# Kernel tuning notes

Measured on AMD Instinct MI355X. Metric: run time of the kernel, lower is better.

The kernel has to match this reference:

```python
import jax, jax.numpy as jnp
import numpy as np

B, T, F = 64, 128, 9            # batch, seq_len, n_feature_fields
N_FEATURES = 32000              # vocab for embedding (N_FEATURES-1 rows) and fc head
EMB = 8
H = 16                          # lstm hidden size
IN0 = (F - 1) * EMB + 1         # lstm layer-0 input size = 65


def setup_inputs() -> dict:
    key = jax.random.key(0)
    ks = jax.random.split(key, 16)
    # x: first F-1 columns are integer-valued categorical indices, last column numeric
    cat = jax.random.randint(ks[0], (B, T, F - 1), 0, N_FEATURES - 1).astype(jnp.float32)
    num = jax.random.normal(ks[1], (B, T, 1), dtype=jnp.float32)
    x = jnp.concatenate([cat, num], axis=-1)
    h0 = jnp.zeros((2, B, H), dtype=jnp.float32)
    c0 = jnp.zeros((2, B, H), dtype=jnp.float32)
    emb = jax.random.normal(ks[2], (N_FEATURES - 1, EMB), dtype=jnp.float32)
    s0 = 1.0 / np.sqrt(IN0)
    s1 = 1.0 / np.sqrt(H)
    W_ih0 = jax.random.normal(ks[3], (4 * H, IN0), dtype=jnp.float32) * s0
    W_hh0 = jax.random.normal(ks[4], (4 * H, H), dtype=jnp.float32) * s1
    b_ih0 = jax.random.normal(ks[5], (4 * H,), dtype=jnp.float32) * 0.1
    b_hh0 = jax.random.normal(ks[6], (4 * H,), dtype=jnp.float32) * 0.1
    W_ih1 = jax.random.normal(ks[7], (4 * H, H), dtype=jnp.float32) * s1
    W_hh1 = jax.random.normal(ks[8], (4 * H, H), dtype=jnp.float32) * s1
    b_ih1 = jax.random.normal(ks[9], (4 * H,), dtype=jnp.float32) * 0.1
    b_hh1 = jax.random.normal(ks[10], (4 * H,), dtype=jnp.float32) * 0.1
    fc_w = jax.random.normal(ks[11], (N_FEATURES, H), dtype=jnp.float32) * (1.0 / np.sqrt(H))
    fc_b = jax.random.normal(ks[12], (N_FEATURES,), dtype=jnp.float32) * 0.1
    return {"x": x, "h0": h0, "c0": c0, "emb": emb,
            "W_ih0": W_ih0, "W_hh0": W_hh0, "b_ih0": b_ih0, "b_hh0": b_hh0,
            "W_ih1": W_ih1, "W_hh1": W_hh1, "b_ih1": b_ih1, "b_hh1": b_hh1,
            "fc_w": fc_w, "fc_b": fc_b}


def _lstm_layer(xs, h0, c0, Wih, Whh, bih, bhh):
    # xs: [B, T, I]; PyTorch gate order: i, f, g, o
    xp = jnp.einsum('bti,gi->btg', xs, Wih) + (bih + bhh)  # [B, T, 4H]
    xp = jnp.swapaxes(xp, 0, 1)  # [T, B, 4H]

    def step(carry, xt):
        h, c = carry
        g = xt + h @ Whh.T
        i, f, gg, o = jnp.split(g, 4, axis=-1)
        c = jax.nn.sigmoid(f) * c + jax.nn.sigmoid(i) * jnp.tanh(gg)
        h = jax.nn.sigmoid(o) * jnp.tanh(c)
        return (h, c), h

    (hT, cT), ys = jax.lax.scan(step, (h0, c0), xp)
    return jnp.swapaxes(ys, 0, 1), hT, cT


def reference(x, h0, c0, emb, W_ih0, W_hh0, b_ih0, b_hh0,
              W_ih1, W_hh1, b_ih1, b_hh1, fc_w, fc_b):
    cat = x[:, :, :-1].astype(jnp.int32)          # [B, T, F-1]
    num = x[:, :, -1:]                            # [B, T, 1]
    e = emb[cat].reshape(x.shape[0], x.shape[1], -1)  # [B, T, (F-1)*EMB]
    inp = jnp.concatenate([e, num], axis=-1)      # [B, T, IN0]
    y0, h0T, c0T = _lstm_layer(inp, h0[0], c0[0], W_ih0, W_hh0, b_ih0, b_hh0)
    y1, h1T, c1T = _lstm_layer(y0, h0[1], c0[1], W_ih1, W_hh1, b_ih1, b_hh1)
    logits = jnp.einsum('bth,vh->btv', y1, fc_w) + fc_b  # [B, T, N_FEATURES]
    hN = jnp.stack([h0T, h1T], axis=0)
    cN = jnp.stack([c0T, c1T], axis=0)
    return logits, hN, cN
```

## Files before the change

kernel.cpp:

```cpp
#include <hip/hip_runtime.h>
#include <math.h>

#define BB 64
#define TT 128
#define HH 16
#define GG 64
#define IN0_ 65
#define VV 32000
#define NROWS (BB*TT)
#define RSTRIDE 68

typedef float f32x4 __attribute__((ext_vector_type(4)));

__device__ __forceinline__ float sigf(float x) {
    return 1.0f / (1.0f + __expf(-x));
}
__device__ __forceinline__ float tanhfast(float x) {
    return 1.0f - 2.0f / (__expf(2.0f * x) + 1.0f);
}
__device__ __forceinline__ float bcast(float v, int lane) {
    return __uint_as_float(__builtin_amdgcn_readlane(__float_as_uint(v), lane));
}

__global__ __launch_bounds__(256) void fused_front(const float* __restrict__ x,
                           const float* __restrict__ emb,
                           const float* __restrict__ Wih0, const float* __restrict__ bih0,
                           const float* __restrict__ bhh0,
                           const float* __restrict__ h0in, const float* __restrict__ c0in,
                           const float* __restrict__ Whh0,
                           const float* __restrict__ Wih1, const float* __restrict__ Whh1,
                           const float* __restrict__ bih1, const float* __restrict__ bhh1,
                           float* __restrict__ y1, float* __restrict__ outTail) {
    __shared__ float insh[TT * RSTRIDE];
    __shared__ float wsh[GG * IN0_];
    const int b   = blockIdx.x;
    const int tid = threadIdx.x;
    const int wave = tid >> 6, g = tid & 63;
    const float* xb = x + (size_t)b * TT * 9;

    for (int i = tid; i < GG * IN0_ / 4; i += 256) {
        float4 wv = *reinterpret_cast<const float4*>(Wih0 + i * 4);
        wsh[i*4+0] = wv.x; wsh[i*4+1] = wv.y; wsh[i*4+2] = wv.z; wsh[i*4+3] = wv.w;
    }
    #pragma unroll
    for (int it = 0; it < 8; ++it) {
        int q = tid + it * 256;
        int p = q >> 1, half = q & 1;
        int r = p >> 3, f = p & 7;
        int idx = (int)xb[r * 9 + f];
        const float* er = emb + (size_t)idx * 8 + half * 4;
        float4 e = *reinterpret_cast<const float4*>(er);
        float* d = &insh[r * RSTRIDE + f * 8 + half * 4];
        d[0] = e.x; d[1] = e.y; d[2] = e.z; d[3] = e.w;
    }
    if (tid < TT) insh[tid * RSTRIDE + 64] = xb[tid * 9 + 8];
    __syncthreads();

    {
        float wreg[IN0_];
        #pragma unroll
        for (int k = 0; k < IN0_; ++k) wreg[k] = wsh[g * IN0_ + k];
        const float bias0 = bih0[g] + bhh0[g];
        for (int r = 0; r < 32; ++r) {
            const int row = wave * 32 + r;
            const float* ir = &insh[row * RSTRIDE];
            float a0 = bias0, a1 = 0.0f, a2 = 0.0f, a3 = 0.0f;
            #pragma unroll
            for (int k4 = 0; k4 < 16; ++k4) {
                f32x4 v = *reinterpret_cast<const f32x4*>(ir + k4 * 4);
                float p0 = v.x * wreg[k4*4+0] + v.y * wreg[k4*4+1]
                         + v.z * wreg[k4*4+2] + v.w * wreg[k4*4+3];
                if ((k4 & 3) == 0) a0 += p0;
                else if ((k4 & 3) == 1) a1 += p0;
                else if ((k4 & 3) == 2) a2 += p0;
                else a3 += p0;
            }
            float acc = (a0 + a1) + (a2 + a3) + ir[64] * wreg[64];
            insh[row * RSTRIDE + g] = acc;
        }
    }
    __syncthreads();

    if (tid >= 64) return;

    const int j = g & 15;
    float w0[HH], wi1[HH], w1[HH];
    #pragma unroll
    for (int k = 0; k < HH; ++k) {
        w0[k]  = Whh0[g * HH + k];
        wi1[k] = Wih1[g * HH + k];
        w1[k]  = Whh1[g * HH + k];
    }
    const float bias1 = bih1[g] + bhh1[g];

    float h0v = h0in[b * HH + j];
    float h1v = h0in[BB * HH + b * HH + j];
    float c0v = c0in[b * HH + j];
    float c1v = c0in[BB * HH + b * HH + j];

    {
        float aa = insh[g], ab = 0.0f;
        #pragma unroll
        for (int k = 0; k < 8; ++k) {
            aa += bcast(h0v, k) * w0[k];
            ab += bcast(h0v, k + 8) * w0[k + 8];
        }
        float acc = aa + ab;
        float iv = __shfl(acc, j), fv = __shfl(acc, j + 16);
        float gv = __shfl(acc, j + 32), ov = __shfl(acc, j + 48);
        c0v = sigf(fv) * c0v + sigf(iv) * tanhfast(gv);
        h0v = sigf(ov) * tanhfast(c0v);
    }

    for (int t = 0; t < TT - 1; ++t) {
        float xpn = insh[(t + 1) * RSTRIDE + g];
        float a1a = bias1, a1b = 0.0f, a1c = 0.0f, a1d = 0.0f;
        float a0a = 0.0f,  a0b = 0.0f;
        #pragma unroll
        for (int k = 0; k < 8; ++k) {
            float h0k  = bcast(h0v, k);
            float h0k8 = bcast(h0v, k + 8);
            float h1k  = bcast(h1v, k);
            float h1k8 = bcast(h1v, k + 8);
            a1a += h0k  * wi1[k];
            a1b += h0k8 * wi1[k + 8];
            a1c += h1k  * w1[k];
            a1d += h1k8 * w1[k + 8];
            a0a += h0k  * w0[k];
            a0b += h0k8 * w0[k + 8];
        }
        float acc1 = (a1a + a1b) + (a1c + a1d);
        float acc0 = xpn + a0a + a0b;
        float iv1 = __shfl(acc1, j), fv1 = __shfl(acc1, j + 16);
        float gv1 = __shfl(acc1, j + 32), ov1 = __shfl(acc1, j + 48);
        float iv0 = __shfl(acc0, j), fv0 = __shfl(acc0, j + 16);
        float gv0 = __shfl(acc0, j + 32), ov0 = __shfl(acc0, j + 48);
        c1v = sigf(fv1) * c1v + sigf(iv1) * tanhfast(gv1);
        h1v = sigf(ov1) * tanhfast(c1v);
        c0v = sigf(fv0) * c0v + sigf(iv0) * tanhfast(gv0);
        h0v = sigf(ov0) * tanhfast(c0v);
        if (g < HH) y1[(size_t)(b * TT + t) * HH + g] = h1v;
    }

    {
        float a1a = bias1, a1b = 0.0f, a1c = 0.0f, a1d = 0.0f;
        #pragma unroll
        for (int k = 0; k < 8; ++k) {
            float h0k  = bcast(h0v, k);
            float h0k8 = bcast(h0v, k + 8);
            float h1k  = bcast(h1v, k);
            float h1k8 = bcast(h1v, k + 8);
            a1a += h0k  * wi1[k];
            a1b += h0k8 * wi1[k + 8];
            a1c += h1k  * w1[k];
            a1d += h1k8 * w1[k + 8];
        }
        float acc1 = (a1a + a1b) + (a1c + a1d);
        float iv1 = __shfl(acc1, j), fv1 = __shfl(acc1, j + 16);
        float gv1 = __shfl(acc1, j + 32), ov1 = __shfl(acc1, j + 48);
        c1v = sigf(fv1) * c1v + sigf(iv1) * tanhfast(gv1);
        h1v = sigf(ov1) * tanhfast(c1v);
        if (g < HH) y1[(size_t)(b * TT + TT - 1) * HH + g] = h1v;
    }

    if (g < HH) {
        outTail[b * HH + g]               = h0v;
        outTail[BB * HH + b * HH + g]     = h1v;
        outTail[2 * BB * HH + b * HH + g] = c0v;
        outTail[3 * BB * HH + b * HH + g] = c1v;
    }
}

__global__ __launch_bounds__(256) void fc_kernel(const float* __restrict__ y1,
                          const float* __restrict__ fcw, const float* __restrict__ fcb,
                          float* __restrict__ out) {
    const int tid  = threadIdx.x;
    const int v0   = blockIdx.x * 1024 + tid * 4;
    const int row0 = blockIdx.y * 32;

    if (v0 >= VV) return;

    float w[4][HH];
    #pragma unroll
    for (int jj = 0; jj < 4; ++jj) {
        const float4* wp = reinterpret_cast<const float4*>(fcw + (size_t)(v0 + jj) * HH);
        float4 a = wp[0], b = wp[1], c = wp[2], d = wp[3];
        w[jj][0]=a.x; w[jj][1]=a.y; w[jj][2]=a.z; w[jj][3]=a.w;
        w[jj][4]=b.x; w[jj][5]=b.y; w[jj][6]=b.z; w[jj][7]=b.w;
        w[jj][8]=c.x; w[jj][9]=c.y; w[jj][10]=c.z; w[jj][11]=c.w;
        w[jj][12]=d.x; w[jj][13]=d.y; w[jj][14]=d.z; w[jj][15]=d.w;
    }
    const float4 bias = *reinterpret_cast<const float4*>(fcb + v0);

    const f32x4* yrow = reinterpret_cast<const f32x4*>(y1 + (size_t)row0 * HH);

    float* orow = out + (size_t)row0 * VV + v0;
    #pragma unroll 4
    for (int r = 0; r < 32; ++r) {
        f32x4 y0 = yrow[r * 4 + 0];
        f32x4 y1v = yrow[r * 4 + 1];
        f32x4 y2 = yrow[r * 4 + 2];
        f32x4 y3 = yrow[r * 4 + 3];
        float a0 = bias.x, a1 = bias.y, a2 = bias.z, a3 = bias.w;
        #pragma unroll
        for (int jj = 0; jj < 4; ++jj) {
            float* wj = w[jj];
            float acc = y0.x*wj[0] + y0.y*wj[1] + y0.z*wj[2] + y0.w*wj[3]
                      + y1v.x*wj[4] + y1v.y*wj[5] + y1v.z*wj[6] + y1v.w*wj[7]
                      + y2.x*wj[8] + y2.y*wj[9] + y2.z*wj[10] + y2.w*wj[11]
                      + y3.x*wj[12] + y3.y*wj[13] + y3.z*wj[14] + y3.w*wj[15];
            if (jj == 0) a0 += acc;
            else if (jj == 1) a1 += acc;
            else if (jj == 2) a2 += acc;
            else a3 += acc;
        }
        f32x4 o;
        o.x = a0; o.y = a1; o.z = a2; o.w = a3;
        __builtin_nontemporal_store(o, reinterpret_cast<f32x4*>(orow));
        orow += VV;
    }
}

extern "C" void kernel_launch(void* const* d_in, const int* in_sizes, int n_in,
                              void* d_out, int out_size, void* d_ws, size_t ws_size,
                              hipStream_t stream) {
    const float* x    = (const float*)d_in[0];
    const float* h0   = (const float*)d_in[1];
    const float* c0   = (const float*)d_in[2];
    const float* emb  = (const float*)d_in[3];
    const float* Wih0 = (const float*)d_in[4];
    const float* Whh0 = (const float*)d_in[5];
    const float* bih0 = (const float*)d_in[6];
    const float* bhh0 = (const float*)d_in[7];
    const float* Wih1 = (const float*)d_in[8];
    const float* Whh1 = (const float*)d_in[9];
    const float* bih1 = (const float*)d_in[10];
    const float* bhh1 = (const float*)d_in[11];
    const float* fcw  = (const float*)d_in[12];
    const float* fcb  = (const float*)d_in[13];

    float* out = (float*)d_out;
    float* y1  = (float*)d_ws;
    float* outTail = out + (size_t)NROWS * VV;

    fused_front<<<BB, 256, 0, stream>>>(x, emb, Wih0, bih0, bhh0, h0, c0,
                                        Whh0, Wih1, Whh1, bih1, bhh1, y1, outTail);
    fc_kernel<<<dim3(32, NROWS / 32), 256, 0, stream>>>(y1, fcw, fcb, out);
}
```

Baseline: 282.5 us.

## Process two batch sequences per block in fused LSTM front kernel

Each block of the fused embedding+LSTM kernel now handles two batch elements instead of one, interleaving their recurrences in a single wave. This gives the serial per-timestep chain independent work to hide readlane/shuffle/transcendental latency. The cost is half as many blocks, doubled LDS via dynamic shared memory (about 86KB), and more registers. Layer-0 input projection work per wave doubles.

New measurement: 346.5 us. 1.23x slower.

```diff
diff --git a/kernel.cpp b/kernel.cpp
--- a/kernel.cpp
+++ b/kernel.cpp
@@ -9,6 +9,7 @@
 #define VV 32000
 #define NROWS (BB*TT)
 #define RSTRIDE 68
+#define BOFF (TT*RSTRIDE)
 
 typedef float f32x4 __attribute__((ext_vector_type(4)));
 
@@ -31,29 +32,29 @@
                            const float* __restrict__ Wih1, const float* __restrict__ Whh1,
                            const float* __restrict__ bih1, const float* __restrict__ bhh1,
                            float* __restrict__ y1, float* __restrict__ outTail) {
-    __shared__ float insh[TT * RSTRIDE];
-    __shared__ float wsh[GG * IN0_];
-    const int b   = blockIdx.x;
+    extern __shared__ float smem[];
+    float* wsh = smem + 2 * BOFF;
+    const int b0  = blockIdx.x * 2;
     const int tid = threadIdx.x;
     const int wave = tid >> 6, g = tid & 63;
-    const float* xb = x + (size_t)b * TT * 9;
+    const float* xg = x + (size_t)b0 * TT * 9;
 
     for (int i = tid; i < GG * IN0_ / 4; i += 256) {
         float4 wv = *reinterpret_cast<const float4*>(Wih0 + i * 4);
         wsh[i*4+0] = wv.x; wsh[i*4+1] = wv.y; wsh[i*4+2] = wv.z; wsh[i*4+3] = wv.w;
     }
     #pragma unroll
-    for (int it = 0; it < 8; ++it) {
+    for (int it = 0; it < 16; ++it) {
         int q = tid + it * 256;
         int p = q >> 1, half = q & 1;
         int r = p >> 3, f = p & 7;
-        int idx = (int)xb[r * 9 + f];
+        int idx = (int)xg[r * 9 + f];
         const float* er = emb + (size_t)idx * 8 + half * 4;
         float4 e = *reinterpret_cast<const float4*>(er);
-        float* d = &insh[r * RSTRIDE + f * 8 + half * 4];
+        float* d = &smem[(r >> 7) * BOFF + (r & 127) * RSTRIDE + f * 8 + half * 4];
         d[0] = e.x; d[1] = e.y; d[2] = e.z; d[3] = e.w;
     }
-    if (tid < TT) insh[tid * RSTRIDE + 64] = xb[tid * 9 + 8];
+    smem[(tid >> 7) * BOFF + (tid & 127) * RSTRIDE + 64] = xg[tid * 9 + 8];
     __syncthreads();
 
     {
@@ -61,9 +62,10 @@
         #pragma unroll
         for (int k = 0; k < IN0_; ++k) wreg[k] = wsh[g * IN0_ + k];
         const float bias0 = bih0[g] + bhh0[g];
-        for (int r = 0; r < 32; ++r) {
-            const int row = wave * 32 + r;
-            const float* ir = &insh[row * RSTRIDE];
+        float* base = smem + (wave >> 1) * BOFF;
+        for (int r = 0; r < 64; ++r) {
+            const int row = (wave & 1) * 64 + r;
+            const float* ir = &base[row * RSTRIDE];
             float a0 = bias0, a1 = 0.0f, a2 = 0.0f, a3 = 0.0f;
             #pragma unroll
             for (int k4 = 0; k4 < 16; ++k4) {
@@ -76,7 +78,7 @@
                 else a3 += p0;
             }
             float acc = (a0 + a1) + (a2 + a3) + ir[64] * wreg[64];
-            insh[row * RSTRIDE + g] = acc;
+            base[row * RSTRIDE + g] = acc;
         }
     }
     __syncthreads();
@@ -92,82 +94,123 @@
         w1[k]  = Whh1[g * HH + k];
     }
     const float bias1 = bih1[g] + bhh1[g];
-
-    float h0v = h0in[b * HH + j];
-    float h1v = h0in[BB * HH + b * HH + j];
-    float c0v = c0in[b * HH + j];
-    float c1v = c0in[BB * HH + b * HH + j];
+    const int bA = b0, bB = b0 + 1;
+
+    float h0A = h0in[bA * HH + j],            h0B = h0in[bB * HH + j];
+    float h1A = h0in[BB * HH + bA * HH + j],  h1B = h0in[BB * HH + bB * HH + j];
+    float c0A = c0in[bA * HH + j],            c0B = c0in[bB * HH + j];
+    float c1A = c0in[BB * HH + bA * HH + j],  c1B = c0in[BB * HH + bB * HH + j];
+
+    const float* xpA = smem;
+    const float* xpB = smem + BOFF;
 
     {
-        float aa = insh[g], ab = 0.0f;
+        float aA = xpA[g], abA = 0.0f, aB = xpB[g], abB = 0.0f;
         #pragma unroll
         for (int k = 0; k < 8; ++k) {
-            aa += bcast(h0v, k) * w0[k];
-            ab += bcast(h0v, k + 8) * w0[k + 8];
-        }
-        float acc = aa + ab;
-        float iv = __shfl(acc, j), fv = __shfl(acc, j + 16);
-        float gv = __shfl(acc, j + 32), ov = __shfl(acc, j + 48);
-        c0v = sigf(fv) * c0v + sigf(iv) * tanhfast(gv);
-        h0v = sigf(ov) * tanhfast(c0v);
+            float wA = w0[k], wB = w0[k + 8];
+            aA  += bcast(h0A, k)     * wA;
+            abA += bcast(h0A, k + 8) * wB;
+            aB  += bcast(h0B, k)     * wA;
+            abB += bcast(h0B, k + 8) * wB;
+        }
+        float accA = aA + abA, accB = aB + abB;
+        float ivA = __shfl(accA, j), fvA = __shfl(accA, j + 16);
+        float gvA = __shfl(accA, j + 32), ovA = __shfl(accA, j + 48);
+        float ivB = __shfl(accB, j), fvB = __shfl(accB, j + 16);
+        float gvB = __shfl(accB, j + 32), ovB = __shfl(accB, j + 48);
+        c0A = sigf(fvA) * c0A + sigf(ivA) * tanhfast(gvA);
+        c0B = sigf(fvB) * c0B + sigf(ivB) * tanhfast(gvB);
+        h0A = sigf(ovA) * tanhfast(c0A);
+        h0B = sigf(ovB) * tanhfast(c0B);
     }
 
     for (int t = 0; t < TT - 1; ++t) {
-        float xpn = insh[(t + 1) * RSTRIDE + g];
-        float a1a = bias1, a1b = 0.0f, a1c = 0.0f, a1d = 0.0f;
-        float a0a = 0.0f,  a0b = 0.0f;
+        float xpnA = xpA[(t + 1) * RSTRIDE + g];
+        float xpnB = xpB[(t + 1) * RSTRIDE + g];
+        float a1aA = bias1, a1bA = 0.0f, a1cA = 0.0f, a1dA = 0.0f;
+        float a0aA = 0.0f,  a0bA = 0.0f;
+        float a1aB = bias1, a1bB = 0.0f, a1cB = 0.0f, a1dB = 0.0f;
+        float a0aB = 0.0f,  a0bB = 0.0f;
         #pragma unroll
         for (int k = 0; k < 8; ++k) {
-            float h0k  = bcast(h0v, k);
-            float h0k8 = bcast(h0v, k + 8);
-            float h1k  = bcast(h1v, k);
-            float h1k8 = bcast(h1v, k + 8);
-            a1a += h0k  * wi1[k];
-            a1b += h0k8 * wi1[k + 8];
-            a1c += h1k  * w1[k];
-            a1d += h1k8 * w1[k + 8];
-            a0a += h0k  * w0[k];
-            a0b += h0k8 * w0[k + 8];
-        }
-        float acc1 = (a1a + a1b) + (a1c + a1d);
-        float acc0 = xpn + a0a + a0b;
-        float iv1 = __shfl(acc1, j), fv1 = __shfl(acc1, j + 16);
-        float gv1 = __shfl(acc1, j + 32), ov1 = __shfl(acc1, j + 48);
-        float iv0 = __shfl(acc0, j), fv0 = __shfl(acc0, j + 16);
-        float gv0 = __shfl(acc0, j + 32), ov0 = __shfl(acc0, j + 48);
-        c1v = sigf(fv1) * c1v + sigf(iv1) * tanhfast(gv1);
-        h1v = sigf(ov1) * tanhfast(c1v);
-        c0v = sigf(fv0) * c0v + sigf(iv0) * tanhfast(gv0);
-        h0v = sigf(ov0) * tanhfast(c0v);
-        if (g < HH) y1[(size_t)(b * TT + t) * HH + g] = h1v;
+            float h0kA  = bcast(h0A, k),     h0k8A = bcast(h0A, k + 8);
+            float h1kA  = bcast(h1A, k),     h1k8A = bcast(h1A, k + 8);
+            float h0kB  = bcast(h0B, k),     h0k8B = bcast(h0B, k + 8);
+            float h1kB  = bcast(h1B, k),     h1k8B = bcast(h1B, k + 8);
+            float wiA = wi1[k], wiB = wi1[k + 8];
+            float whA = w1[k],  whB = w1[k + 8];
+            float w0a = w0[k],  w0b = w0[k + 8];
+            a1aA += h0kA  * wiA;  a1bA += h0k8A * wiB;
+            a1cA += h1kA  * whA;  a1dA += h1k8A * whB;
+            a0aA += h0kA  * w0a;  a0bA += h0k8A * w0b;
+            a1aB += h0kB  * wiA;  a1bB += h0k8B * wiB;
+            a1cB += h1kB  * whA;  a1dB += h1k8B * whB;
+            a0aB += h0kB  * w0a;  a0bB += h0k8B * w0b;
+        }
+        float acc1A = (a1aA + a1bA) + (a1cA + a1dA);
+        float acc0A = xpnA + a0aA + a0bA;
+        float acc1B = (a1aB + a1bB) + (a1cB + a1dB);
+        float acc0B = xpnB + a0aB + a0bB;
+        float iv1A = __shfl(acc1A, j), fv1A = __shfl(acc1A, j + 16);
+        float gv1A = __shfl(acc1A, j + 32), ov1A = __shfl(acc1A, j + 48);
+        float iv0A = __shfl(acc0A, j), fv0A = __shfl(acc0A, j + 16);
+        float gv0A = __shfl(acc0A, j + 32), ov0A = __shfl(acc0A, j + 48);
+        float iv1B = __shfl(acc1B, j), fv1B = __shfl(acc1B, j + 16);
+        float gv1B = __shfl(acc1B, j + 32), ov1B = __shfl(acc1B, j + 48);
+        float iv0B = __shfl(acc0B, j), fv0B = __shfl(acc0B, j + 16);
+        float gv0B = __shfl(acc0B, j + 32), ov0B = __shfl(acc0B, j + 48);
+        c1A = sigf(fv1A) * c1A + sigf(iv1A) * tanhfast(gv1A);
+        c1B = sigf(fv1B) * c1B + sigf(iv1B) * tanhfast(gv1B);
+        h1A = sigf(ov1A) * tanhfast(c1A);
+        h1B = sigf(ov1B) * tanhfast(c1B);
+        c0A = sigf(fv0A) * c0A + sigf(iv0A) * tanhfast(gv0A);
+        c0B = sigf(fv0B) * c0B + sigf(iv0B) * tanhfast(gv0B);
+        h0A = sigf(ov0A) * tanhfast(c0A);
+        h0B = sigf(ov0B) * tanhfast(c0B);
+        if (g < HH) {
+            y1[(size_t)(bA * TT + t) * HH + g] = h1A;
+            y1[(size_t)(bB * TT + t) * HH + g] = h1B;
+        }
     }
 
     {
-        float a1a = bias1, a1b = 0.0f, a1c = 0.0f, a1d = 0.0f;
+        float a1aA = bias1, a1bA = 0.0f, a1cA = 0.0f, a1dA = 0.0f;
+        float a1aB = bias1, a1bB = 0.0f, a1cB = 0.0f, a1dB = 0.0f;
         #pragma unroll
         for (int k = 0; k < 8; ++k) {
-            float h0k  = bcast(h0v, k);
-            float h0k8 = bcast(h0v, k + 8);
-            float h1k  = bcast(h1v, k);
-            float h1k8 = bcast(h1v, k + 8);
-            a1a += h0k  * wi1[k];
-            a1b += h0k8 * wi1[k + 8];
-            a1c += h1k  * w1[k];
-            a1d += h1k8 * w1[k + 8];
-        }
-        float acc1 = (a1a + a1b) + (a1c + a1d);
-        float iv1 = __shfl(acc1, j), fv1 = __shfl(acc1, j + 16);
-        float gv1 = __shfl(acc1, j + 32), ov1 = __shfl(acc1, j + 48);
-        c1v = sigf(fv1) * c1v + sigf(iv1) * tanhfast(gv1);
-        h1v = sigf(ov1) * tanhfast(c1v);
-        if (g < HH) y1[(size_t)(b * TT + TT - 1) * HH + g] = h1v;
+            float wiA = wi1[k], wiB = wi1[k + 8];
+            float whA = w1[k],  whB = w1[k + 8];
+            a1aA += bcast(h0A, k)     * wiA;  a1bA += bcast(h0A, k + 8) * wiB;
+            a1cA += bcast(h1A, k)     * whA;  a1dA += bcast(h1A, k + 8) * whB;
+            a1aB += bcast(h0B, k)     * wiA;  a1bB += bcast(h0B, k + 8) * wiB;
+            a1cB += bcast(h1B, k)     * whA;  a1dB += bcast(h1B, k + 8) * whB;
+        }
+        float acc1A = (a1aA + a1bA) + (a1cA + a1dA);
+        float acc1B = (a1aB + a1bB) + (a1cB + a1dB);
+        float iv1A = __shfl(acc1A, j), fv1A = __shfl(acc1A, j + 16);
+        float gv1A = __shfl(acc1A, j + 32), ov1A = __shfl(acc1A, j + 48);
+        float iv1B = __shfl(acc1B, j), fv1B = __shfl(acc1B, j + 16);
+        float gv1B = __shfl(acc1B, j + 32), ov1B = __shfl(acc1B, j + 48);
+        c1A = sigf(fv1A) * c1A + sigf(iv1A) * tanhfast(gv1A);
+        c1B = sigf(fv1B) * c1B + sigf(iv1B) * tanhfast(gv1B);
+        h1A = sigf(ov1A) * tanhfast(c1A);
+        h1B = sigf(ov1B) * tanhfast(c1B);
+        if (g < HH) {
+            y1[(size_t)(bA * TT + TT - 1) * HH + g] = h1A;
+            y1[(size_t)(bB * TT + TT - 1) * HH + g] = h1B;
+        }
     }
 
     if (g < HH) {
-        outTail[b * HH + g]               = h0v;
-        outTail[BB * HH + b * HH + g]     = h1v;
-        outTail[2 * BB * HH + b * HH + g] = c0v;
-        outTail[3 * BB * HH + b * HH + g] = c1v;
+        outTail[bA * HH + g]               = h0A;
+        outTail[bB * HH + g]               = h0B;
+        outTail[BB * HH + bA * HH + g]     = h1A;
+        outTail[BB * HH + bB * HH + g]     = h1B;
+        outTail[2 * BB * HH + bA * HH + g] = c0A;
+        outTail[2 * BB * HH + bB * HH + g] = c0B;
+        outTail[3 * BB * HH + bA * HH + g] = c1A;
+        outTail[3 * BB * HH + bB * HH + g] = c1B;
     }
 }
 
@@ -243,7 +286,8 @@
     float* y1  = (float*)d_ws;
     float* outTail = out + (size_t)NROWS * VV;
 
-    fused_front<<<BB, 256, 0, stream>>>(x, emb, Wih0, bih0, bhh0, h0, c0,
+    const size_t lds_bytes = (2 * BOFF + GG * IN0_) * sizeof(float);
+    fused_front<<<BB / 2, 256, lds_bytes, stream>>>(x, emb, Wih0, bih0, bhh0, h0, c0,
                                         Whh0, Wih1, Whh1, bih1, bhh1, y1, outTail);
     fc_kernel<<<dim3(32, NROWS / 32), 256, 0, stream>>>(y1, fcw, fcb, out);
 }
```

## Split the two LSTM layers across two waves with shared-memory handoff

Applied to the files above, without the earlier changes.

Shrinks the front kernel block to 128 threads. Wave 0 runs layer 0 and computes the layer-1 input projection; wave 1 runs the layer-1 recurrence, reading that projection from a double-buffered shared array. The goal is to spread the per-step matvec work across two waves instead of one. In exchange it adds a block barrier every timestep and halves the threads available for the embedding and input-projection phase.

Measured after the change: 269.6 us. 4.6% less time.

```diff
diff --git a/kernel.cpp b/kernel.cpp
--- a/kernel.cpp
+++ b/kernel.cpp
@@ -22,7 +22,7 @@
     return __uint_as_float(__builtin_amdgcn_readlane(__float_as_uint(v), lane));
 }
 
-__global__ __launch_bounds__(256) void fused_front(const float* __restrict__ x,
+__global__ __launch_bounds__(128) void fused_front(const float* __restrict__ x,
                            const float* __restrict__ emb,
                            const float* __restrict__ Wih0, const float* __restrict__ bih0,
                            const float* __restrict__ bhh0,
@@ -33,18 +33,19 @@
                            float* __restrict__ y1, float* __restrict__ outTail) {
     __shared__ float insh[TT * RSTRIDE];
     __shared__ float wsh[GG * IN0_];
+    __shared__ float z1buf[2][GG];
     const int b   = blockIdx.x;
     const int tid = threadIdx.x;
     const int wave = tid >> 6, g = tid & 63;
     const float* xb = x + (size_t)b * TT * 9;
 
-    for (int i = tid; i < GG * IN0_ / 4; i += 256) {
+    for (int i = tid; i < GG * IN0_ / 4; i += 128) {
         float4 wv = *reinterpret_cast<const float4*>(Wih0 + i * 4);
         wsh[i*4+0] = wv.x; wsh[i*4+1] = wv.y; wsh[i*4+2] = wv.z; wsh[i*4+3] = wv.w;
     }
     #pragma unroll
-    for (int it = 0; it < 8; ++it) {
-        int q = tid + it * 256;
+    for (int it = 0; it < 16; ++it) {
+        int q = tid + it * 128;
         int p = q >> 1, half = q & 1;
         int r = p >> 3, f = p & 7;
         int idx = (int)xb[r * 9 + f];
@@ -53,7 +54,7 @@
         float* d = &insh[r * RSTRIDE + f * 8 + half * 4];
         d[0] = e.x; d[1] = e.y; d[2] = e.z; d[3] = e.w;
     }
-    if (tid < TT) insh[tid * RSTRIDE + 64] = xb[tid * 9 + 8];
+    insh[tid * RSTRIDE + 64] = xb[tid * 9 + 8];
     __syncthreads();
 
     {
@@ -61,8 +62,8 @@
         #pragma unroll
         for (int k = 0; k < IN0_; ++k) wreg[k] = wsh[g * IN0_ + k];
         const float bias0 = bih0[g] + bhh0[g];
-        for (int r = 0; r < 32; ++r) {
-            const int row = wave * 32 + r;
+        for (int r = 0; r < 64; ++r) {
+            const int row = wave * 64 + r;
             const float* ir = &insh[row * RSTRIDE];
             float a0 = bias0, a1 = 0.0f, a2 = 0.0f, a3 = 0.0f;
             #pragma unroll
@@ -81,93 +82,64 @@
     }
     __syncthreads();
 
-    if (tid >= 64) return;
-
     const int j = g & 15;
-    float w0[HH], wi1[HH], w1[HH];
+    float wa[HH], wb[HH];
     #pragma unroll
     for (int k = 0; k < HH; ++k) {
-        w0[k]  = Whh0[g * HH + k];
-        wi1[k] = Wih1[g * HH + k];
-        w1[k]  = Whh1[g * HH + k];
+        wa[k] = (wave == 0) ? Whh0[g * HH + k] : Whh1[g * HH + k];
+        wb[k] = (wave == 0) ? Wih1[g * HH + k] : 0.0f;
     }
     const float bias1 = bih1[g] + bhh1[g];
 
-    float h0v = h0in[b * HH + j];
-    float h1v = h0in[BB * HH + b * HH + j];
-    float c0v = c0in[b * HH + j];
-    float c1v = c0in[BB * HH + b * HH + j];
-
-    {
-        float aa = insh[g], ab = 0.0f;
-        #pragma unroll
-        for (int k = 0; k < 8; ++k) {
-            aa += bcast(h0v, k) * w0[k];
-            ab += bcast(h0v, k + 8) * w0[k + 8];
-        }
-        float acc = aa + ab;
-        float iv = __shfl(acc, j), fv = __shfl(acc, j + 16);
-        float gv = __shfl(acc, j + 32), ov = __shfl(acc, j + 48);
-        c0v = sigf(fv) * c0v + sigf(iv) * tanhfast(gv);
-        h0v = sigf(ov) * tanhfast(c0v);
-    }
-
-    for (int t = 0; t < TT - 1; ++t) {
-        float xpn = insh[(t + 1) * RSTRIDE + g];
-        float a1a = bias1, a1b = 0.0f, a1c = 0.0f, a1d = 0.0f;
-        float a0a = 0.0f,  a0b = 0.0f;
-        #pragma unroll
-        for (int k = 0; k < 8; ++k) {
-            float h0k  = bcast(h0v, k);
-            float h0k8 = bcast(h0v, k + 8);
-            float h1k  = bcast(h1v, k);
-            float h1k8 = bcast(h1v, k + 8);
-            a1a += h0k  * wi1[k];
-            a1b += h0k8 * wi1[k + 8];
-            a1c += h1k  * w1[k];
-            a1d += h1k8 * w1[k + 8];
-            a0a += h0k  * w0[k];
-            a0b += h0k8 * w0[k + 8];
-        }
-        float acc1 = (a1a + a1b) + (a1c + a1d);
-        float acc0 = xpn + a0a + a0b;
-        float iv1 = __shfl(acc1, j), fv1 = __shfl(acc1, j + 16);
-        float gv1 = __shfl(acc1, j + 32), ov1 = __shfl(acc1, j + 48);
-        float iv0 = __shfl(acc0, j), fv0 = __shfl(acc0, j + 16);
-        float gv0 = __shfl(acc0, j + 32), ov0 = __shfl(acc0, j + 48);
-        c1v = sigf(fv1) * c1v + sigf(iv1) * tanhfast(gv1);
-        h1v = sigf(ov1) * tanhfast(c1v);
-        c0v = sigf(fv0) * c0v + sigf(iv0) * tanhfast(gv0);
-        h0v = sigf(ov0) * tanhfast(c0v);
-        if (g < HH) y1[(size_t)(b * TT + t) * HH + g] = h1v;
-    }
-
-    {
-        float a1a = bias1, a1b = 0.0f, a1c = 0.0f, a1d = 0.0f;
-        #pragma unroll
-        for (int k = 0; k < 8; ++k) {
-            float h0k  = bcast(h0v, k);
-            float h0k8 = bcast(h0v, k + 8);
-            float h1k  = bcast(h1v, k);
-            float h1k8 = bcast(h1v, k + 8);
-            a1a += h0k  * wi1[k];
-            a1b += h0k8 * wi1[k + 8];
-            a1c += h1k  * w1[k];
-            a1d += h1k8 * w1[k + 8];
-        }
-        float acc1 = (a1a + a1b) + (a1c + a1d);
-        float iv1 = __shfl(acc1, j), fv1 = __shfl(acc1, j + 16);
-        float gv1 = __shfl(acc1, j + 32), ov1 = __shfl(acc1, j + 48);
-        c1v = sigf(fv1) * c1v + sigf(iv1) * tanhfast(gv1);
-        h1v = sigf(ov1) * tanhfast(c1v);
-        if (g < HH) y1[(size_t)(b * TT + TT - 1) * HH + g] = h1v;
+    float hv = (wave == 0) ? h0in[b * HH + j] : h0in[BB * HH + b * HH + j];
+    float cv = (wave == 0) ? c0in[b * HH + j] : c0in[BB * HH + b * HH + j];
+
+    for (int t = 0; t < TT; ++t) {
+        if (wave == 0) {
+            float aa = insh[t * RSTRIDE + g], ab = 0.0f;
+            #pragma unroll
+            for (int k = 0; k < 8; ++k) {
+                aa += bcast(hv, k) * wa[k];
+                ab += bcast(hv, k + 8) * wa[k + 8];
+            }
+            float acc = aa + ab;
+            float iv = __shfl(acc, j), fv = __shfl(acc, j + 16);
+            float gv = __shfl(acc, j + 32), ov = __shfl(acc, j + 48);
+            cv = sigf(fv) * cv + sigf(iv) * tanhfast(gv);
+            hv = sigf(ov) * tanhfast(cv);
+            float za = 0.0f, zb = 0.0f;
+            #pragma unroll
+            for (int k = 0; k < 8; ++k) {
+                za += bcast(hv, k) * wb[k];
+                zb += bcast(hv, k + 8) * wb[k + 8];
+            }
+            z1buf[t & 1][g] = za + zb;
+        }
+        __syncthreads();
+        if (wave == 1) {
+            float aa = bias1 + z1buf[t & 1][g], ab = 0.0f;
+            #pragma unroll
+            for (int k = 0; k < 8; ++k) {
+                aa += bcast(hv, k) * wa[k];
+                ab += bcast(hv, k + 8) * wa[k + 8];
+            }
+            float acc = aa + ab;
+            float iv = __shfl(acc, j), fv = __shfl(acc, j + 16);
+            float gv = __shfl(acc, j + 32), ov = __shfl(acc, j + 48);
+            cv = sigf(fv) * cv + sigf(iv) * tanhfast(gv);
+            hv = sigf(ov) * tanhfast(cv);
+            if (g < HH) y1[(size_t)(b * TT + t) * HH + g] = hv;
+        }
     }
 
     if (g < HH) {
-        outTail[b * HH + g]               = h0v;
-        outTail[BB * HH + b * HH + g]     = h1v;
-        outTail[2 * BB * HH + b * HH + g] = c0v;
-        outTail[3 * BB * HH + b * HH + g] = c1v;
+        if (wave == 0) {
+            outTail[b * HH + g]               = hv;
+            outTail[2 * BB * HH + b * HH + g] = cv;
+        } else {
+            outTail[BB * HH + b * HH + g]     = hv;
+            outTail[3 * BB * HH + b * HH + g] = cv;
+        }
     }
 }
 
@@ -243,7 +215,7 @@
     float* y1  = (float*)d_ws;
     float* outTail = out + (size_t)NROWS * VV;
 
-    fused_front<<<BB, 256, 0, stream>>>(x, emb, Wih0, bih0, bhh0, h0, c0,
+    fused_front<<<BB, 128, 0, stream>>>(x, emb, Wih0, bih0, bhh0, h0, c0,
                                         Whh0, Wih1, Whh1, bih1, bhh1, y1, outTail);
     fc_kernel<<<dim3(32, NROWS / 32), 256, 0, stream>>>(y1, fcw, fcb, out);
 }
```
